# Kernel tuning notes

Hardware: AMD Instinct MI355X
Metric: run time of the kernel (lower is better)

The kernel has to match this reference:

```python
import jax, jax.numpy as jnp
import numpy as np


def _lstm_dir(x_tbd, Wx, Wh, b, reverse):
    # x_tbd: [T, B, D]; Wx: [D, 4H]; Wh: [H, 4H]; b: [4H]
    if reverse:
        x_tbd = x_tbd[::-1]
    pre = jnp.einsum('tbd,dk->tbk', x_tbd, Wx) + b  # precompute input projection
    T, B, _ = x_tbd.shape
    H = Wh.shape[0]
    init = (jnp.zeros((B, H), x_tbd.dtype), jnp.zeros((B, H), x_tbd.dtype))

    def step(carry, zt):
        c, h = carry
        z = zt + h @ Wh  # [B, 4H]
        i, f, g, o = jnp.split(z, 4, axis=-1)
        i = jax.nn.sigmoid(i)
        f = jax.nn.sigmoid(f)
        g = jnp.tanh(g)
        o = jax.nn.sigmoid(o)
        c = f * c + i * g
        h = o * jnp.tanh(c)
        return (c, h), h

    _, hs = jax.lax.scan(step, init, pre)  # hs: [T, B, H]
    if reverse:
        hs = hs[::-1]
    return hs


def _bilstm(x, layers):
    # x: [B, T, D] batch-major -> time-major
    x = jnp.swapaxes(x, 0, 1)  # [T, B, D]
    for (Wxf, Whf, bf, Wxb, Whb, bb) in layers:
        hf = _lstm_dir(x, Wxf, Whf, bf, reverse=False)
        hb = _lstm_dir(x, Wxb, Whb, bb, reverse=True)
        x = jnp.concatenate([hf, hb], axis=-1)  # [T, B, 2H]
    return jnp.swapaxes(x, 0, 1)  # [B, T, 2H]


def setup_inputs() -> dict:
    key = jax.random.key(0)
    B, T, D, H = 8, 2048, 512, 512
    ks = jax.random.split(key, 9)
    s_in = 1.0 / np.sqrt(D)
    s_h = 1.0 / np.sqrt(H)
    s_in2 = 1.0 / np.sqrt(2 * H)
    return {
        'x': jax.random.normal(ks[0], (B, T, D), jnp.float32),
        'Wx0f': jax.random.normal(ks[1], (D, 4 * H), jnp.float32) * s_in,
        'Wh0f': jax.random.normal(ks[2], (H, 4 * H), jnp.float32) * s_h,
        'b0f': jnp.zeros((4 * H,), jnp.float32),
        'Wx0b': jax.random.normal(ks[3], (D, 4 * H), jnp.float32) * s_in,
        'Wh0b': jax.random.normal(ks[4], (H, 4 * H), jnp.float32) * s_h,
        'b0b': jnp.zeros((4 * H,), jnp.float32),
        'Wx1f': jax.random.normal(ks[5], (2 * H, 4 * H), jnp.float32) * s_in2,
        'Wh1f': jax.random.normal(ks[6], (H, 4 * H), jnp.float32) * s_h,
        'b1f': jnp.zeros((4 * H,), jnp.float32),
        'Wx1b': jax.random.normal(ks[7], (2 * H, 4 * H), jnp.float32) * s_in2,
        'Wh1b': jax.random.normal(ks[8], (H, 4 * H), jnp.float32) * s_h,
        'b1b': jnp.zeros((4 * H,), jnp.float32),
    }


def reference(x, Wx0f, Wh0f, b0f, Wx0b, Wh0b, b0b, Wx1f, Wh1f, b1f, Wx1b, Wh1b, b1b):
    layers = [
        (Wx0f, Wh0f, b0f, Wx0b, Wh0b, b0b),
        (Wx1f, Wh1f, b1f, Wx1b, Wh1b, b1b),
    ]
    return _bilstm(x, layers)
```

## Files before the change

kernel.cpp:

```cpp
#include <hip/hip_runtime.h>
#include <hip/hip_bf16.h>
#include <stdint.h>

typedef unsigned short u16;
typedef unsigned int   u32;
typedef unsigned long long u64;
typedef __attribute__((ext_vector_type(8))) short short8;
typedef __attribute__((ext_vector_type(4))) float f32x4;

#define T_SEQ 2048
#define NTOK  16384
#define NGATE 4096

__device__ __forceinline__ u16 f2bf(float f) {
    u32 u = __builtin_bit_cast(u32, f);
    return (u16)((u + 0x7fffu + ((u >> 16) & 1u)) >> 16);
}
__device__ __forceinline__ float bf2f(u16 s) {
    return __builtin_bit_cast(float, (u32)s << 16);
}

__global__ void k_init(u32* comm, int n_comm) {
    int i = blockIdx.x * blockDim.x + threadIdx.x;
    int stride = gridDim.x * blockDim.x;
    for (int k = i; k < n_comm; k += stride) comm[k] = 0u;
}

__global__ void k_f2bf(const float* __restrict__ src, u16* __restrict__ dst, int n4) {
    int i = blockIdx.x * blockDim.x + threadIdx.x;
    if (i >= n4) return;
    float4 v = ((const float4*)src)[i];
    u32 lo = (u32)f2bf(v.x) | ((u32)f2bf(v.y) << 16);
    u32 hi = (u32)f2bf(v.z) | ((u32)f2bf(v.w) << 16);
    ((uint2*)dst)[i] = make_uint2(lo, hi);
}

__global__ void k_pack_wxT(const float* __restrict__ Wf, const float* __restrict__ Wb,
                           u16* __restrict__ dst, int K, int klog ) {
    int gid = blockIdx.x * blockDim.x + threadIdx.x;
    if (gid >= (NGATE << klog)) return;
    int n  = gid >> klog;
    int kc = gid & ((1 << klog) - 1);
    int dir = n >> 11, pcol = n & 2047;
    int c = pcol >> 4, uu = (pcol >> 2) & 3, g = pcol & 3;
    int u = c * 4 + uu;
    int oc = g * 512 + u;
    const float* src = dir ? Wb : Wf;
    u16* d = dst + (size_t)n * K + kc * 8;
    #pragma unroll
    for (int j = 0; j < 8; j++) d[j] = f2bf(src[(size_t)(kc * 8 + j) * 2048 + oc]);
}

__global__ void k_pack_whF(const float* __restrict__ Whf, const float* __restrict__ Whb,
                           u16* __restrict__ dst) {
    int gid = blockIdx.x * blockDim.x + threadIdx.x;
    int lane = gid & 63, kk = (gid >> 6) & 15, c = (gid >> 10) & 127, dir = (gid >> 17) & 1;
    int col16 = lane & 15, uu = col16 >> 2, g = col16 & 3;
    int u = c * 4 + uu, oc = g * 512 + u;
    int kbase = kk * 32 + (lane >> 4) * 8;
    const float* src = dir ? Whb : Whf;
    u16* d = dst + (size_t)gid * 8;
    #pragma unroll
    for (int j = 0; j < 8; j++) d[j] = f2bf(src[(size_t)(kbase + j) * 2048 + oc]);
}

template <int K>
__global__ __launch_bounds__(256) void k_gemm(const u16* __restrict__ A,
                                              const u16* __restrict__ BT,
                                              u16* __restrict__ C) {
    __shared__ __align__(16) u16 a_lds[128][72];
    __shared__ __align__(16) u16 b_lds[128][72];
    const int tid = threadIdx.x;
    const int lane = tid & 63;
    const int wav = tid >> 6;
    const int wr = wav >> 1, wc = wav & 1;
    const int row0 = blockIdx.y * 128, col0 = blockIdx.x * 128;
    const int r_ld = lane & 15;
    const int k_ld = (lane >> 4) * 8;
    f32x4 acc[4][4] = {};
    for (int kt = 0; kt < K; kt += 64) {
        __syncthreads();
        #pragma unroll
        for (int it = 0; it < 4; it++) {
            int cc = tid + it * 256;
            int r = cc >> 3, ko = (cc & 7) * 8;
            *(short8*)&a_lds[r][ko] = *(const short8*)&A[(size_t)(row0 + r) * K + kt + ko];
            *(short8*)&b_lds[r][ko] = *(const short8*)&BT[(size_t)(col0 + r) * K + kt + ko];
        }
        __syncthreads();
        #pragma unroll
        for (int kk = 0; kk < 2; kk++) {
            short8 af[4], bfr[4];
            #pragma unroll
            for (int m = 0; m < 4; m++)
                af[m] = *(const short8*)&a_lds[wr * 64 + m * 16 + r_ld][kk * 32 + k_ld];
            #pragma unroll
            for (int n = 0; n < 4; n++)
                bfr[n] = *(const short8*)&b_lds[wc * 64 + n * 16 + r_ld][kk * 32 + k_ld];
            #pragma unroll
            for (int m = 0; m < 4; m++)
                #pragma unroll
                for (int n = 0; n < 4; n++)
                    acc[m][n] = __builtin_amdgcn_mfma_f32_16x16x32_bf16(af[m], bfr[n], acc[m][n], 0, 0, 0);
        }
    }
    const int rrow = (lane >> 4) * 4;
    const int rcol = lane & 15;
    #pragma unroll
    for (int m = 0; m < 4; m++)
        #pragma unroll
        for (int n = 0; n < 4; n++) {
            size_t rbase = (size_t)(row0 + wr * 64 + m * 16 + rrow);
            int col = col0 + wc * 64 + n * 16 + rcol;
            #pragma unroll
            for (int r = 0; r < 4; r++)
                C[(rbase + r) * NGATE + col] = f2bf(acc[m][n][r]);
        }
}

__global__ __launch_bounds__(512) void k_scan(
    const u16* __restrict__ pre,
    const u16* __restrict__ whF,
    const float* __restrict__ bias_f, const float* __restrict__ bias_b,
    u16* __restrict__ y_bf,
    float* __restrict__ y_f32,
    u32* __restrict__ comm)
{
    __shared__ __align__(16) u16   h_lds[2][8][520];
    __shared__ __align__(16) u16   z_pre[2][8][264];
    __shared__ __align__(16) float z_mm[2][8][260];

    const int tid = threadIdx.x;
    const int dir = (int)(blockIdx.x >> 3);
    const int p   = (int)(blockIdx.x & 7);
    const int l   = tid & 63;
    const int w   = tid >> 6;

    short8 bfrag[2][16];
    #pragma unroll
    for (int q = 0; q < 2; q++) {
        const u16* base = whF + ((size_t)(dir * 128 + p * 16 + 2 * w + q) * 16) * 512 + (size_t)l * 8;
        #pragma unroll
        for (int kk = 0; kk < 16; kk++) bfrag[q][kk] = *(const short8*)(base + kk * 512);
    }

    float c_st = 0.f;
    const int gj  = tid & 63;
    const int u_g = p * 64 + gj;
    const float* bias = dir ? bias_b : bias_f;
    const float bi  = bias[u_g];        const float bff = bias[512 + u_g];
    const float bg  = bias[1024 + u_g]; const float bo  = bias[1536 + u_g];

    const int a_b = l & 7;
    const int a_k = (l >> 4) * 8;
    const int zr  = l >> 4;

    u32* const cb32 = comm + (size_t)dir * 8192;
    u64* const cbU  = (u64*)cb32;
    const int u2    = (2 * tid) & 511;
    const int b0    = tid >> 8;
    const bool own  = (u2 >> 6) == p;

    h_lds[0][w][u_g] = 0;

    const int pr_b = tid >> 5, pr_seg = tid & 31;
    short8 preg;
    if (tid < 256) {
        const int t0 = dir ? (T_SEQ - 1) : 0;
        preg = *(const short8*)&pre[((size_t)pr_b * T_SEQ + t0) * NGATE + dir * 2048 + p * 256 + pr_seg * 8];
    }

    for (int s = 0; s < T_SEQ; s++) {
        const int t  = dir ? (T_SEQ - 1 - s) : s;
        const int hb = s & 1;
        if (!own) {
            const u64* sb = cbU + (size_t)((s + 1) & 1) * 2048;
            const u32 want = (u32)s & 0xffffu;
            u64 v0 = 0, v1 = 0, v2 = 0, v3 = 0;
            bool d0 = false, d1 = false, d2 = false, d3 = false;
            auto tagok = [&](u64 v) {
                return (((u32)(v >> 16) & 0xffffu) == want) & ((u32)(v >> 48) == want);
            };
            int spins = 0;
            for (;;) {
                if (!d0) { v0 = __hip_atomic_load(&sb[tid],        __ATOMIC_RELAXED, __HIP_MEMORY_SCOPE_AGENT); d0 = tagok(v0); }
                if (!d1) { v1 = __hip_atomic_load(&sb[tid + 512],  __ATOMIC_RELAXED, __HIP_MEMORY_SCOPE_AGENT); d1 = tagok(v1); }
                if (!d2) { v2 = __hip_atomic_load(&sb[tid + 1024], __ATOMIC_RELAXED, __HIP_MEMORY_SCOPE_AGENT); d2 = tagok(v2); }
                if (!d3) { v3 = __hip_atomic_load(&sb[tid + 1536], __ATOMIC_RELAXED, __HIP_MEMORY_SCOPE_AGENT); d3 = tagok(v3); }
                if (d0 & d1 & d2 & d3) break;
                if (spins++) __builtin_amdgcn_s_sleep(1);
            }
            auto pk = [](u64 v) { return ((u32)v & 0xffffu) | ((u32)(v >> 32) << 16); };
            *(u32*)&h_lds[hb][b0 + 0][u2] = pk(v0);
            *(u32*)&h_lds[hb][b0 + 2][u2] = pk(v1);
            *(u32*)&h_lds[hb][b0 + 4][u2] = pk(v2);
            *(u32*)&h_lds[hb][b0 + 6][u2] = pk(v3);
        }
        if (tid < 256) {
            *(short8*)&z_pre[hb][pr_b][pr_seg * 8] = preg;
            if (s + 1 < T_SEQ) {
                const int t2 = dir ? (T_SEQ - 2 - s) : (s + 1);
                preg = *(const short8*)&pre[((size_t)pr_b * T_SEQ + t2) * NGATE + dir * 2048 + p * 256 + pr_seg * 8];
            }
        }
        __syncthreads();
        {
            f32x4 acc0 = {}, acc1 = {};
            #pragma unroll
            for (int kk = 0; kk < 16; kk++) {
                short8 a = *(const short8*)&h_lds[hb][a_b][kk * 32 + a_k];
                acc0 = __builtin_amdgcn_mfma_f32_16x16x32_bf16(a, bfrag[0][kk], acc0, 0, 0, 0);
                acc1 = __builtin_amdgcn_mfma_f32_16x16x32_bf16(a, bfrag[1][kk], acc1, 0, 0, 0);
            }
            if (zr < 2) {
                #pragma unroll
                for (int r = 0; r < 4; r++) {
                    z_mm[hb][zr * 4 + r][(2 * w + 0) * 16 + (l & 15)] = acc0[r];
                    z_mm[hb][zr * 4 + r][(2 * w + 1) * 16 + (l & 15)] = acc1[r];
                }
            }
        }
        __syncthreads();
        {
            float4 z4 = *(const float4*)&z_mm[hb][w][4 * gj];
            u64 pz    = *(const u64*)&z_pre[hb][w][4 * gj];
            float zi = z4.x + bf2f((u16)pz)         + bi;
            float zf = z4.y + bf2f((u16)(pz >> 16)) + bff;
            float zg = z4.z + bf2f((u16)(pz >> 32)) + bg;
            float zo = z4.w + bf2f((u16)(pz >> 48)) + bo;
            float ig = 1.f / (1.f + __expf(-zi));
            float fg = 1.f / (1.f + __expf(-zf));
            float gg = 2.f / (1.f + __expf(-2.f * zg)) - 1.f;
            float og = 1.f / (1.f + __expf(-zo));
            c_st = fg * c_st + ig * gg;
            float th = 2.f / (1.f + __expf(-2.f * c_st)) - 1.f;
            float hv = og * th;
            u16 hb16 = f2bf(hv);
            __hip_atomic_store(&cb32[(size_t)(s & 1) * 4096 + w * 512 + u_g],
                               (u32)hb16 | ((u32)((s + 1) & 0xffff) << 16),
                               __ATOMIC_RELAXED, __HIP_MEMORY_SCOPE_AGENT);
            h_lds[(s + 1) & 1][w][u_g] = hb16;
            size_t rr = (size_t)w * T_SEQ + t;
            if (y_bf) y_bf[rr * 1024 + dir * 512 + u_g] = hb16;
            else      y_f32[rr * 1024 + dir * 512 + u_g] = hv;
        }
    }
}

extern "C" void kernel_launch(void* const* d_in, const int* in_sizes, int n_in,
                              void* d_out, int out_size, void* d_ws, size_t ws_size,
                              hipStream_t stream) {
    const float* x    = (const float*)d_in[0];
    const float* Wx0f = (const float*)d_in[1];
    const float* Wh0f = (const float*)d_in[2];
    const float* b0f  = (const float*)d_in[3];
    const float* Wx0b = (const float*)d_in[4];
    const float* Wh0b = (const float*)d_in[5];
    const float* b0b  = (const float*)d_in[6];
    const float* Wx1f = (const float*)d_in[7];
    const float* Wh1f = (const float*)d_in[8];
    const float* b1f  = (const float*)d_in[9];
    const float* Wx1b = (const float*)d_in[10];
    const float* Wh1b = (const float*)d_in[11];
    const float* b1b  = (const float*)d_in[12];
    float* out = (float*)d_out;

    char* ws = (char*)d_ws;
    size_t off = 0;
    auto take = [&](size_t bytes) {
        char* pp = ws + off;
        off = (off + bytes + 255) & ~(size_t)255;
        return pp;
    };
    u16* pre  = (u16*)take((size_t)NTOK * NGATE * 2);
    u16* x_bf = (u16*)take((size_t)NTOK * 512 * 2);
    u16* y0   = (u16*)take((size_t)NTOK * 1024 * 2);
    u16* wxT0 = (u16*)take((size_t)NGATE * 512 * 2);
    u16* wxT1 = (u16*)take((size_t)NGATE * 1024 * 2);
    u16* whF  = (u16*)take((size_t)2 * 2097152 * 2);
    u32* comm = (u32*)take((size_t)4 * 8192 * 4);

    k_init<<<32, 256, 0, stream>>>(comm, 4 * 8192);
    k_f2bf<<<8192, 256, 0, stream>>>(x, x_bf, NTOK * 512 / 4);
    k_pack_wxT<<<1024, 256, 0, stream>>>(Wx0f, Wx0b, wxT0, 512, 6);
    k_pack_wxT<<<2048, 256, 0, stream>>>(Wx1f, Wx1b, wxT1, 1024, 7);
    k_pack_whF<<<1024, 256, 0, stream>>>(Wh0f, Wh0b, whF);
    k_pack_whF<<<1024, 256, 0, stream>>>(Wh1f, Wh1b, whF + 2097152);

    k_gemm<512><<<dim3(32, 128), 256, 0, stream>>>(x_bf, wxT0, pre);
    k_scan<<<16, 512, 0, stream>>>(pre, whF, b0f, b0b, y0, nullptr, comm);
    k_gemm<1024><<<dim3(32, 128), 256, 0, stream>>>(y0, wxT1, pre);
    k_scan<<<16, 512, 0, stream>>>(pre, whF + 2097152, b1f, b1b, nullptr, out,
                                   comm + 2 * 8192);
}
```

Before: 11.32 ms.

## Remap LSTM gate ownership so each wave consumes its own MFMA output, dropping a barrier

Each wave now writes its MFMA gate tile to a private LDS slot and then computes the cell update for the same 8 hidden units across all 8 batch rows. This lets the second __syncthreads per timestep be removed, shortening the serial per-step critical path of the recurrent scan. The comm buffer indexing and the polling layout are remapped to match the new unit/batch ownership. The cost is a different LDS access pattern for the gate reads, and correctness now depends on each wave's read-after-write within its own slot being ordered without a barrier.

```diff
diff --git a/kernel.cpp b/kernel.cpp
--- a/kernel.cpp
+++ b/kernel.cpp
@@ -128,7 +128,7 @@
 {
     __shared__ __align__(16) u16   h_lds[2][8][520];
     __shared__ __align__(16) u16   z_pre[2][8][264];
-    __shared__ __align__(16) float z_mm[2][8][260];
+    __shared__ __align__(16) float z_mm[8][8][36];
 
     const int tid = threadIdx.x;
     const int dir = (int)(blockIdx.x >> 3);
@@ -144,9 +144,11 @@
         for (int kk = 0; kk < 16; kk++) bfrag[q][kk] = *(const short8*)(base + kk * 512);
     }
 
+    const int b_g  = l >> 3;
+    const int u16g = l & 7;
+    const int ub   = 8 * w + u16g;
+    const int u_g  = p * 64 + ub;
     float c_st = 0.f;
-    const int gj  = tid & 63;
-    const int u_g = p * 64 + gj;
     const float* bias = dir ? bias_b : bias_f;
     const float bi  = bias[u_g];        const float bff = bias[512 + u_g];
     const float bg  = bias[1024 + u_g]; const float bo  = bias[1536 + u_g];
@@ -154,14 +156,14 @@
     const int a_b = l & 7;
     const int a_k = (l >> 4) * 8;
     const int zr  = l >> 4;
+    const int c16 = l & 15;
 
     u32* const cb32 = comm + (size_t)dir * 8192;
-    u64* const cbU  = (u64*)cb32;
-    const int u2    = (2 * tid) & 511;
-    const int b0    = tid >> 8;
-    const bool own  = (u2 >> 6) == p;
-
-    h_lds[0][w][u_g] = 0;
+    const int up   = tid & 255;
+    const int bhi  = tid >> 8;
+    const bool own = (up >> 5) == p;
+
+    h_lds[0][tid >> 6][p * 64 + (tid & 63)] = 0;
 
     const int pr_b = tid >> 5, pr_seg = tid & 31;
     short8 preg;
@@ -174,27 +176,31 @@
         const int t  = dir ? (T_SEQ - 1 - s) : s;
         const int hb = s & 1;
         if (!own) {
-            const u64* sb = cbU + (size_t)((s + 1) & 1) * 2048;
+            const u64* sb = (const u64*)(cb32 + (size_t)((s + 1) & 1) * 4096);
             const u32 want = (u32)s & 0xffffu;
             u64 v0 = 0, v1 = 0, v2 = 0, v3 = 0;
             bool d0 = false, d1 = false, d2 = false, d3 = false;
             auto tagok = [&](u64 v) {
                 return (((u32)(v >> 16) & 0xffffu) == want) & ((u32)(v >> 48) == want);
             };
+            const u64* a0p = &sb[(2 * 0 + bhi) * 256 + up];
+            const u64* a1p = &sb[(2 * 1 + bhi) * 256 + up];
+            const u64* a2p = &sb[(2 * 2 + bhi) * 256 + up];
+            const u64* a3p = &sb[(2 * 3 + bhi) * 256 + up];
             int spins = 0;
             for (;;) {
-                if (!d0) { v0 = __hip_atomic_load(&sb[tid],        __ATOMIC_RELAXED, __HIP_MEMORY_SCOPE_AGENT); d0 = tagok(v0); }
-                if (!d1) { v1 = __hip_atomic_load(&sb[tid + 512],  __ATOMIC_RELAXED, __HIP_MEMORY_SCOPE_AGENT); d1 = tagok(v1); }
-                if (!d2) { v2 = __hip_atomic_load(&sb[tid + 1024], __ATOMIC_RELAXED, __HIP_MEMORY_SCOPE_AGENT); d2 = tagok(v2); }
-                if (!d3) { v3 = __hip_atomic_load(&sb[tid + 1536], __ATOMIC_RELAXED, __HIP_MEMORY_SCOPE_AGENT); d3 = tagok(v3); }
+                if (!d0) { v0 = __hip_atomic_load(a0p, __ATOMIC_RELAXED, __HIP_MEMORY_SCOPE_AGENT); d0 = tagok(v0); }
+                if (!d1) { v1 = __hip_atomic_load(a1p, __ATOMIC_RELAXED, __HIP_MEMORY_SCOPE_AGENT); d1 = tagok(v1); }
+                if (!d2) { v2 = __hip_atomic_load(a2p, __ATOMIC_RELAXED, __HIP_MEMORY_SCOPE_AGENT); d2 = tagok(v2); }
+                if (!d3) { v3 = __hip_atomic_load(a3p, __ATOMIC_RELAXED, __HIP_MEMORY_SCOPE_AGENT); d3 = tagok(v3); }
                 if (d0 & d1 & d2 & d3) break;
                 if (spins++) __builtin_amdgcn_s_sleep(1);
             }
             auto pk = [](u64 v) { return ((u32)v & 0xffffu) | ((u32)(v >> 32) << 16); };
-            *(u32*)&h_lds[hb][b0 + 0][u2] = pk(v0);
-            *(u32*)&h_lds[hb][b0 + 2][u2] = pk(v1);
-            *(u32*)&h_lds[hb][b0 + 4][u2] = pk(v2);
-            *(u32*)&h_lds[hb][b0 + 6][u2] = pk(v3);
+            *(u32*)&h_lds[hb][2 * 0 + bhi][2 * up] = pk(v0);
+            *(u32*)&h_lds[hb][2 * 1 + bhi][2 * up] = pk(v1);
+            *(u32*)&h_lds[hb][2 * 2 + bhi][2 * up] = pk(v2);
+            *(u32*)&h_lds[hb][2 * 3 + bhi][2 * up] = pk(v3);
         }
         if (tid < 256) {
             *(short8*)&z_pre[hb][pr_b][pr_seg * 8] = preg;
@@ -215,15 +221,14 @@
             if (zr < 2) {
                 #pragma unroll
                 for (int r = 0; r < 4; r++) {
-                    z_mm[hb][zr * 4 + r][(2 * w + 0) * 16 + (l & 15)] = acc0[r];
-                    z_mm[hb][zr * 4 + r][(2 * w + 1) * 16 + (l & 15)] = acc1[r];
+                    z_mm[w][zr * 4 + r][c16]      = acc0[r];
+                    z_mm[w][zr * 4 + r][16 + c16] = acc1[r];
                 }
             }
         }
-        __syncthreads();
         {
-            float4 z4 = *(const float4*)&z_mm[hb][w][4 * gj];
-            u64 pz    = *(const u64*)&z_pre[hb][w][4 * gj];
+            float4 z4 = *(const float4*)&z_mm[w][b_g][4 * u16g];
+            u64 pz    = *(const u64*)&z_pre[hb][b_g][4 * ub];
             float zi = z4.x + bf2f((u16)pz)         + bi;
             float zf = z4.y + bf2f((u16)(pz >> 16)) + bff;
             float zg = z4.z + bf2f((u16)(pz >> 32)) + bg;
@@ -236,11 +241,11 @@
             float th = 2.f / (1.f + __expf(-2.f * c_st)) - 1.f;
             float hv = og * th;
             u16 hb16 = f2bf(hv);
-            __hip_atomic_store(&cb32[(size_t)(s & 1) * 4096 + w * 512 + u_g],
+            __hip_atomic_store(&cb32[(size_t)(s & 1) * 4096 + b_g * 512 + u_g],
                                (u32)hb16 | ((u32)((s + 1) & 0xffff) << 16),
                                __ATOMIC_RELAXED, __HIP_MEMORY_SCOPE_AGENT);
-            h_lds[(s + 1) & 1][w][u_g] = hb16;
-            size_t rr = (size_t)w * T_SEQ + t;
+            h_lds[(s + 1) & 1][b_g][u_g] = hb16;
+            size_t rr = (size_t)b_g * T_SEQ + t;
             if (y_bf) y_bf[rr * 1024 + dir * 512 + u_g] = hb16;
             else      y_f32[rr * 1024 + dir * 512 + u_g] = hv;
         }
```

Measured after the change: 12.04 ms. 6.3% more time.
